# Optimization experiments

Measured on AMD Instinct MI355X. Metric: run time of the kernel, lower is better.

Reference implementation:

```python
import jax, jax.numpy as jnp
import numpy as np

S, O, J, B = 16, 8, 32, 4096
HID, OUT_HID = 240, 512
P1, P2 = 0.5, 0.65  # Bayesian (concrete) dropout probabilities, mid of [0.5, 0.8]


def setup_inputs() -> dict:
    key = jax.random.key(0)
    ks = jax.random.split(key, 20)
    sc = 0.05
    return {
        "y_t": jax.random.normal(ks[0], (B, O), jnp.float32),
        "x_filtered_prev": jax.random.normal(ks[1], (B, S), jnp.float32),
        "F": jax.random.normal(ks[2], (S, S), jnp.float32) * sc,
        "H": jax.random.normal(ks[3], (O, S), jnp.float32) * sc,
        "W_fc_in": jax.random.normal(ks[4], (HID, 2 * S + 2 * O), jnp.float32) * sc,
        "b_fc_in": jax.random.normal(ks[5], (HID,), jnp.float32) * sc,
        "W_ih": jax.random.normal(ks[6], (3 * HID, HID), jnp.float32) * sc,
        "W_hh": jax.random.normal(ks[7], (3 * HID, HID), jnp.float32) * sc,
        "b_ih": jax.random.normal(ks[8], (3 * HID,), jnp.float32) * sc,
        "b_hh": jax.random.normal(ks[9], (3 * HID,), jnp.float32) * sc,
        "W_out1": jax.random.normal(ks[10], (OUT_HID, HID), jnp.float32) * sc,
        "b_out1": jax.random.normal(ks[11], (OUT_HID,), jnp.float32) * sc,
        "W_out2": jax.random.normal(ks[12], (S * O, OUT_HID), jnp.float32) * sc,
        "b_out2": jax.random.normal(ks[13], (S * O,), jnp.float32) * sc,
        "h_init": jax.random.normal(ks[14], (HID,), jnp.float32),
        "u1": jax.random.uniform(ks[15], (J, B, HID), jnp.float32),
        "u2": jax.random.uniform(ks[16], (J, B, OUT_HID), jnp.float32),
    }


def reference(y_t, x_filtered_prev, F, H, W_fc_in, b_fc_in, W_ih, W_hh, b_ih,
              b_hh, W_out1, b_out1, W_out2, b_out2, h_init, u1, u2):
    # --- first step of step_StateBayesianKalmanNet, fully batched over (J, B) ---
    x_pred = x_filtered_prev @ F.T                 # f(x): [B,S]
    y_pred = x_pred @ H.T                          # h(x): [B,O]
    state_inno = x_filtered_prev - x_pred          # x_filt_prev - x_pred_prev
    innovation = y_t - y_pred
    diff_state = jnp.zeros_like(x_filtered_prev)   # first step: x_prev - x_prev_prev = 0
    diff_obs = y_t - y_pred                        # y_prev = h(x_pred) on first step

    feats = jnp.concatenate([state_inno, innovation, diff_state, diff_obs], -1)  # [B,48]
    x_in = jax.nn.relu(feats @ W_fc_in.T + b_fc_in)                              # [B,HID]
    mask1 = (u1 > P1).astype(x_in.dtype) / (1.0 - P1)                            # [J,B,HID]
    x_in = x_in[None] * mask1                                                    # Bayesian dropout sample j

    # single GRU cell step (torch gate order r,z,n), h_prev = h_init broadcast
    gx = x_in @ W_ih.T + b_ih                                                    # [J,B,3H]
    gh = h_init @ W_hh.T + b_hh                                                  # [3H]
    xr, xz, xn = jnp.split(gx, 3, axis=-1)
    hr, hz, hn = jnp.split(gh, 3, axis=-1)
    r = jax.nn.sigmoid(xr + hr)
    z = jax.nn.sigmoid(xz + hz)
    n = jnp.tanh(xn + r * hn)
    h_new = (1.0 - z) * n + z * h_init                                           # [J,B,HID]

    o1 = jax.nn.relu(h_new @ W_out1.T + b_out1)                                  # [J,B,OUT_HID]
    mask2 = (u2 > P2).astype(o1.dtype) / (1.0 - P2)
    o1 = o1 * mask2
    K_vec = o1 @ W_out2.T + b_out2                                               # [J,B,S*O]
    K = K_vec.reshape(J, B, S, O)

    correction = jnp.einsum('jbso,bo->jbs', K, innovation)
    x_filt = x_pred[None] + correction                                           # [J,B,S]
    ensemble = jnp.transpose(x_filt, (1, 0, 2))                                  # [B,J,S]
    final_x = ensemble.mean(axis=1)
    final_P_diag = ensemble.var(axis=1, ddof=1)                                  # torch unbiased var

    # concrete-dropout regularization (entropy of the two dropout gates, mean over J)
    reg = -(P1 * jnp.log(P1) + (1 - P1) * jnp.log(1 - P1)) \
          - (P2 * jnp.log(P2) + (1 - P2) * jnp.log(1 - P2))
    reg = jnp.asarray(reg, final_x.dtype)

    return final_x, final_P_diag, reg, ensemble
```

## Files before the change

kernel.cpp:

```cpp
#include <hip/hip_runtime.h>
#include <hip/hip_bf16.h>
#include <math.h>

#define S_DIM 16
#define O_DIM 8
#define J_DIM 32
#define B_DIM 4096
#define HID 240
#define OHID 512

typedef __attribute__((ext_vector_type(8))) short bf16x8;
typedef __attribute__((ext_vector_type(4))) float f32x4;
#define MFMA16(a,b,c) __builtin_amdgcn_mfma_f32_16x16x32_bf16((a),(b),(c),0,0,0)

static __device__ __forceinline__ float fast_rcp(float x) { return __builtin_amdgcn_rcpf(x); }
static __device__ __forceinline__ float fast_sigmoid(float x) {
    return fast_rcp(1.0f + __expf(-x));
}
static __device__ __forceinline__ float fast_tanh(float x) {
    float t = __expf(2.0f * x);
    return 1.0f - 2.0f * fast_rcp(t + 1.0f);
}

#define WS_XPRED   0
#define WS_INNO    (WS_XPRED + B_DIM*S_DIM)
#define WS_FEATS   (WS_INNO + B_DIM*O_DIM)
#define WS_XIN0    (WS_FEATS + B_DIM*48)
#define WS_GH      (WS_XIN0 + B_DIM*HID)
#define WS_WB_OFF  ((WS_GH + 960) * 4)

#define OUT_X      0
#define OUT_P      (B_DIM*S_DIM)
#define OUT_REG    (2*B_DIM*S_DIM)
#define OUT_ENS    (2*B_DIM*S_DIM + 1)

__global__ void k_aux_pre(const float* __restrict__ W_ih, const float* __restrict__ W_hh,
                          const float* __restrict__ b_ih, const float* __restrict__ b_hh,
                          const float* __restrict__ h_init,
                          const float* __restrict__ W_o1, const float* __restrict__ W_o2,
                          __hip_bfloat16* __restrict__ Wihb, __hip_bfloat16* __restrict__ Wo1b,
                          __hip_bfloat16* __restrict__ Wo2b, float* __restrict__ ghb,
                          const float* __restrict__ y, const float* __restrict__ xprev,
                          const float* __restrict__ F, const float* __restrict__ Hm,
                          float* __restrict__ x_pred, float* __restrict__ inno,
                          float* __restrict__ feats)
{
    __shared__ float sF[256], sH[128];
    const int tid = threadIdx.x;
    if (blockIdx.x < 1536) {
        int t = blockIdx.x * 256 + tid;
        if (t < 196608) {
            int e = t & 7, l = (t >> 3) & 15, q = (t >> 7) & 3;
            int ks = (t >> 9) & 7, tile = t >> 12;
            int row = tile*16 + l, col = ks*32 + q*8 + e;
            float v = (row < 720 && col < 240) ? W_ih[row*240 + col] : 0.0f;
            Wihb[t] = __float2bfloat16(v);
        } else if (t < 196608 + 131072) {
            int u = t - 196608;
            int e = u & 7, l = (u >> 3) & 15, q = (u >> 7) & 3;
            int ks = (u >> 9) & 7, tile = u >> 12;
            int row = tile*16 + l, col = ks*32 + q*8 + e;
            float v = (col < 240) ? W_o1[row*240 + col] : 0.0f;
            Wo1b[u] = __float2bfloat16(v);
        } else if (t < 393216) {
            int u = t - 327680;
            int e = u & 7, l = (u >> 3) & 15, q = (u >> 7) & 3;
            int ks = (u >> 9) & 15, tile = u >> 13;
            int row = tile*16 + l, col = ks*32 + q*8 + e;
            Wo2b[u] = __float2bfloat16(W_o2[row*512 + col]);
        }
        if (t < 720) {
            float a = b_hh[t];
            const float* wr = W_hh + t*240;
            for (int k = 0; k < 240; k++) a = fmaf(h_init[k], wr[k], a);
            if (t < 480) {
                ghb[t] = b_ih[t] + a;
            } else {
                ghb[t] = b_ih[t];
                ghb[t + 240] = a;
            }
        }
        return;
    }
    sF[tid] = F[tid];
    if (tid < 128) sH[tid] = Hm[tid];
    __syncthreads();
    int b = (blockIdx.x - 1536) * 256 + tid;
    float xf[16], xp[16], inn[8];
    #pragma unroll
    for (int s = 0; s < 16; s++) xf[s] = xprev[b*16 + s];
    #pragma unroll
    for (int s = 0; s < 16; s++) {
        float a = 0.f;
        #pragma unroll
        for (int k = 0; k < 16; k++) a = fmaf(xf[k], sF[s*16 + k], a);
        xp[s] = a;
    }
    #pragma unroll
    for (int o = 0; o < 8; o++) {
        float a = 0.f;
        #pragma unroll
        for (int k = 0; k < 16; k++) a = fmaf(xp[k], sH[o*16 + k], a);
        inn[o] = y[b*8 + o] - a;
    }
    #pragma unroll
    for (int s = 0; s < 16; s++) x_pred[b*16 + s] = xp[s];
    #pragma unroll
    for (int o = 0; o < 8; o++) inno[b*8 + o] = inn[o];
    float* fb = feats + b*48;
    #pragma unroll
    for (int s = 0; s < 16; s++) fb[s] = xf[s] - xp[s];
    #pragma unroll
    for (int o = 0; o < 8; o++) fb[16 + o] = inn[o];
    #pragma unroll
    for (int s = 0; s < 16; s++) fb[24 + s] = 0.f;
    #pragma unroll
    for (int o = 0; o < 8; o++) fb[40 + o] = inn[o];
}

__global__ void k_pre_b(const float* __restrict__ feats, const float* __restrict__ Wfc,
                        const float* __restrict__ bfc, float* __restrict__ x_in0)
{
    int t = blockIdx.x * 256 + threadIdx.x;
    int b = t / 240, h = t - b*240;
    const float* fb = feats + b*48;
    const float* wr = Wfc + h*48;
    float a = bfc[h];
    #pragma unroll
    for (int k = 0; k < 48; k += 4) {
        const float4 f4 = *(const float4*)&fb[k];
        const float4 w4 = *(const float4*)&wr[k];
        a = fmaf(f4.x, w4.x, fmaf(f4.y, w4.y, fmaf(f4.z, w4.z, fmaf(f4.w, w4.w, a))));
    }
    x_in0[t] = fmaxf(a, 0.f);
}

#define XS_STRIDE 264
#define O1_STRIDE 520

__global__ __launch_bounds__(512, 2) void k_main(
    const float* __restrict__ x_in0, const float* __restrict__ u1,
    const float* __restrict__ u2,
    const __hip_bfloat16* __restrict__ Wihb, const float* __restrict__ ghb,
    const float* __restrict__ h_init,
    const __hip_bfloat16* __restrict__ Wo1b, const float* __restrict__ b_out1,
    const __hip_bfloat16* __restrict__ Wo2b, const float* __restrict__ b_out2,
    const float* __restrict__ x_pred, const float* __restrict__ inno,
    float* __restrict__ ens)
{
    __shared__ __align__(16) char smem[73728];
    __hip_bfloat16* Xs  = (__hip_bfloat16*)smem;
    __hip_bfloat16* Hs  = (__hip_bfloat16*)(smem + 33792);
    __hip_bfloat16* O1s = (__hip_bfloat16*)smem;
    unsigned int* Mbits = (unsigned int*)(smem + 67584);
    float* InnoS = (float*)(smem + 71680);

    const int tid = threadIdx.x;
    const int j  = blockIdx.x >> 6;
    const int b0 = (blockIdx.x & 63) << 6;

    {
        const float4* u2t = (const float4*)(u2 + ((size_t)(j*B_DIM + b0) << 9));
        const int sh = (tid & 7) * 4;
        #pragma unroll
        for (int it = 0; it < 16; ++it) {
            float4 q = u2t[tid + 512*it];
            unsigned int nib = (q.x > 0.65f ? 1u : 0u) | (q.y > 0.65f ? 2u : 0u)
                             | (q.z > 0.65f ? 4u : 0u) | (q.w > 0.65f ? 8u : 0u);
            unsigned int v = nib << sh;
            v |= __shfl_xor(v, 1);
            v |= __shfl_xor(v, 2);
            v |= __shfl_xor(v, 4);
            if ((tid & 7) == 0) Mbits[(tid >> 3) + 64*it] = v;
        }
    }

    {
        const float4* xt = (const float4*)(x_in0 + b0*240);
        const float4* ut = (const float4*)(u1 + (size_t)(j*B_DIM + b0)*240);
        #pragma unroll
        for (int it = 0; it < 8; ++it) {
            int idx = tid + 512*it;
            if (idx < 3840) {
                float4 xv = xt[idx];
                float4 uv = ut[idx];
                int i = idx / 60;
                int h = (idx - i*60) * 4;
                __align__(8) __hip_bfloat16 o[4];
                o[0] = __float2bfloat16(uv.x > 0.5f ? 2.0f*xv.x : 0.0f);
                o[1] = __float2bfloat16(uv.y > 0.5f ? 2.0f*xv.y : 0.0f);
                o[2] = __float2bfloat16(uv.z > 0.5f ? 2.0f*xv.z : 0.0f);
                o[3] = __float2bfloat16(uv.w > 0.5f ? 2.0f*xv.w : 0.0f);
                *(uint2*)&Xs[i*XS_STRIDE + h] = *(const uint2*)o;
            }
        }
    }
    if (tid < 256) {
        int row = tid >> 2, c = 240 + ((tid & 3) << 2);
        uint2 z = {0u, 0u};
        *(uint2*)&Xs[row*XS_STRIDE + c] = z;
        *(uint2*)&Hs[row*XS_STRIDE + c] = z;
    }
    InnoS[tid & 511] = inno[b0*8 + (tid & 511)];
    __syncthreads();

    const int wave = tid >> 6;
    const int l15  = tid & 15;
    const int quad = (tid >> 4) & 3;
    const f32x4 zero4 = {0.f, 0.f, 0.f, 0.f};
    const int fragoff = quad*128 + l15*8;

    #pragma unroll 1
    for (int sl = 0; sl < 2; ++sl) {
        const int t = wave + 8*sl;
        if (t < 15) {
            f32x4 aR[4], aZ[4], aN[4];
            #pragma unroll
            for (int m = 0; m < 4; ++m) { aR[m] = zero4; aZ[m] = zero4; aN[m] = zero4; }

            const __hip_bfloat16* wr = Wihb + t*4096 + fragoff;
            #pragma unroll
            for (int ks = 0; ks < 8; ++ks) {
                const int ko = ks*32 + quad*8;
                bf16x8 a[4];
                #pragma unroll
                for (int m = 0; m < 4; ++m)
                    a[m] = *(const bf16x8*)&Xs[(m*16 + l15)*XS_STRIDE + ko];
                bf16x8 br = *(const bf16x8*)&wr[ks*512];
                bf16x8 bz = *(const bf16x8*)&wr[61440 + ks*512];
                bf16x8 bn = *(const bf16x8*)&wr[122880 + ks*512];
                #pragma unroll
                for (int m = 0; m < 4; ++m) {
                    aR[m] = MFMA16(a[m], br, aR[m]);
                    aZ[m] = MFMA16(a[m], bz, aZ[m]);
                    aN[m] = MFMA16(a[m], bn, aN[m]);
                }
            }
            const int h = t*16 + l15;
            const float add_r = ghb[h],       add_z = ghb[240 + h];
            const float add_n = ghb[480 + h], mul_n = ghb[720 + h];
            const float hi = h_init[h];
            #pragma unroll
            for (int m = 0; m < 4; ++m)
                #pragma unroll
                for (int r = 0; r < 4; ++r) {
                    const int row = m*16 + quad*4 + r;
                    float rg = fast_sigmoid(aR[m][r] + add_r);
                    float zg = fast_sigmoid(aZ[m][r] + add_z);
                    float ng = fast_tanh(aN[m][r] + add_n + rg*mul_n);
                    Hs[row*XS_STRIDE + h] = __float2bfloat16(fmaf(zg, hi - ng, ng));
                }
        }
    }
    __syncthreads();

    {
        f32x4 acc2[4][4];
        #pragma unroll
        for (int it = 0; it < 4; ++it)
            #pragma unroll
            for (int m = 0; m < 4; ++m) acc2[it][m] = zero4;

        const __hip_bfloat16* w2 = Wo1b + wave*16384 + fragoff;
        #pragma unroll
        for (int ks = 0; ks < 8; ++ks) {
            bf16x8 a[4];
            const int ko = ks*32 + quad*8;
            #pragma unroll
            for (int m = 0; m < 4; ++m)
                a[m] = *(const bf16x8*)&Hs[(m*16 + l15)*XS_STRIDE + ko];
            #pragma unroll
            for (int it = 0; it < 4; ++it) {
                bf16x8 b = *(const bf16x8*)&w2[it*4096 + ks*512];
                #pragma unroll
                for (int m = 0; m < 4; ++m)
                    acc2[it][m] = MFMA16(a[m], b, acc2[it][m]);
            }
        }
        __syncthreads();
        const float inv35 = 1.0f/0.35f;
        #pragma unroll
        for (int it = 0; it < 4; ++it) {
            const int n = (wave*4 + it)*16 + l15;
            const float bb = b_out1[n];
            const int wbase = (wave*4 + it) >> 1;
            const int bitpos = ((it & 1) << 4) | l15;
            #pragma unroll
            for (int m = 0; m < 4; ++m)
                #pragma unroll
                for (int r = 0; r < 4; ++r) {
                    const int row = m*16 + quad*4 + r;
                    unsigned int mw = Mbits[row*16 + wbase];
                    float o = fmaxf(acc2[it][m][r] + bb, 0.0f);
                    o = ((mw >> bitpos) & 1u) ? o*inv35 : 0.0f;
                    O1s[row*O1_STRIDE + n] = __float2bfloat16(o);
                }
        }
    }
    __syncthreads();

    {
        const int n = wave*16 + l15;
        const float bo = b_out2[n];
        f32x4 acc3[4];
        #pragma unroll
        for (int m = 0; m < 4; ++m) { f32x4 v = {bo, bo, bo, bo}; acc3[m] = v; }

        const __hip_bfloat16* w3 = Wo2b + wave*8192 + fragoff;
        #pragma unroll
        for (int ks = 0; ks < 16; ++ks) {
            const int ko = ks*32 + quad*8;
            bf16x8 b = *(const bf16x8*)&w3[ks*512];
            #pragma unroll
            for (int m = 0; m < 4; ++m) {
                bf16x8 a = *(const bf16x8*)&O1s[(m*16 + l15)*O1_STRIDE + ko];
                acc3[m] = MFMA16(a, b, acc3[m]);
            }
        }
        const int s = n >> 3, o = n & 7;
        #pragma unroll
        for (int m = 0; m < 4; ++m)
            #pragma unroll
            for (int r = 0; r < 4; ++r) {
                const int row = m*16 + quad*4 + r;
                float v = acc3[m][r] * InnoS[row*8 + o];
                v += __shfl_xor(v, 1);
                v += __shfl_xor(v, 2);
                v += __shfl_xor(v, 4);
                if (o == 0)
                    ens[((b0 + row)*J_DIM + j)*16 + s] = x_pred[(b0 + row)*16 + s] + v;
            }
    }
}

__global__ void k_final(const float* __restrict__ ens, float* __restrict__ out)
{
    int t = blockIdx.x * 256 + threadIdx.x;
    int b = t >> 4, s = t & 15;
    float v[32];
    #pragma unroll
    for (int jj = 0; jj < 32; jj++) v[jj] = ens[(b*32 + jj)*16 + s];
    float m = 0.f;
    #pragma unroll
    for (int jj = 0; jj < 32; jj++) m += v[jj];
    m *= (1.0f/32.0f);
    float var = 0.f;
    #pragma unroll
    for (int jj = 0; jj < 32; jj++) { float d = v[jj] - m; var = fmaf(d, d, var); }
    var *= (1.0f/31.0f);
    out[OUT_X + t] = m;
    out[OUT_P + t] = var;
    if (t == 0) out[OUT_REG] = 1.3405938195945778f;
}

extern "C" void kernel_launch(void* const* d_in, const int* in_sizes, int n_in,
                              void* d_out, int out_size, void* d_ws, size_t ws_size,
                              hipStream_t stream)
{
    (void)in_sizes; (void)n_in; (void)out_size; (void)ws_size;
    const float* y_t    = (const float*)d_in[0];
    const float* xprev  = (const float*)d_in[1];
    const float* F      = (const float*)d_in[2];
    const float* Hm     = (const float*)d_in[3];
    const float* Wfc    = (const float*)d_in[4];
    const float* bfc    = (const float*)d_in[5];
    const float* W_ih   = (const float*)d_in[6];
    const float* W_hh   = (const float*)d_in[7];
    const float* b_ih   = (const float*)d_in[8];
    const float* b_hh   = (const float*)d_in[9];
    const float* W_o1   = (const float*)d_in[10];
    const float* b_o1   = (const float*)d_in[11];
    const float* W_o2   = (const float*)d_in[12];
    const float* b_o2   = (const float*)d_in[13];
    const float* h_init = (const float*)d_in[14];
    const float* u1     = (const float*)d_in[15];
    const float* u2     = (const float*)d_in[16];

    float* out = (float*)d_out;
    float* ws  = (float*)d_ws;
    float* x_pred = ws + WS_XPRED;
    float* inno   = ws + WS_INNO;
    float* feats  = ws + WS_FEATS;
    float* x_in0  = ws + WS_XIN0;
    float* ghb    = ws + WS_GH;
    __hip_bfloat16* Wihb = (__hip_bfloat16*)((char*)d_ws + WS_WB_OFF);
    __hip_bfloat16* Wo1b = Wihb + 768*256;
    __hip_bfloat16* Wo2b = Wo1b + 512*256;
    float* ens    = out + OUT_ENS;

    k_aux_pre<<<dim3(1552), dim3(256), 0, stream>>>(W_ih, W_hh, b_ih, b_hh, h_init,
                                                    W_o1, W_o2, Wihb, Wo1b, Wo2b, ghb,
                                                    y_t, xprev, F, Hm, x_pred, inno, feats);
    k_pre_b<<<dim3(3840), dim3(256), 0, stream>>>(feats, Wfc, bfc, x_in0);
    k_main<<<dim3(2048), dim3(512), 0, stream>>>(x_in0, u1, u2, Wihb, ghb, h_init,
                                                 Wo1b, b_o1, Wo2b, b_o2,
                                                 x_pred, inno, ens);
    k_final<<<dim3(256), dim3(256), 0, stream>>>(ens, out);
}
```

Baseline: 753.8 us.

## Pre-pack dropout masks into bitmasks in a separate kernel and store x_in as bf16

```diff
diff --git a/kernel.cpp b/kernel.cpp
--- a/kernel.cpp
+++ b/kernel.cpp
@@ -25,9 +25,8 @@
 #define WS_XPRED   0
 #define WS_INNO    (WS_XPRED + B_DIM*S_DIM)
 #define WS_FEATS   (WS_INNO + B_DIM*O_DIM)
-#define WS_XIN0    (WS_FEATS + B_DIM*48)
-#define WS_GH      (WS_XIN0 + B_DIM*HID)
-#define WS_WB_OFF  ((WS_GH + 960) * 4)
+#define WS_GH      (WS_FEATS + B_DIM*48)
+#define WS_BYTE    ((WS_GH + 960) * 4)
 
 #define OUT_X      0
 #define OUT_P      (B_DIM*S_DIM)
@@ -119,7 +118,7 @@
 }
 
 __global__ void k_pre_b(const float* __restrict__ feats, const float* __restrict__ Wfc,
-                        const float* __restrict__ bfc, float* __restrict__ x_in0)
+                        const float* __restrict__ bfc, __hip_bfloat16* __restrict__ xb)
 {
     int t = blockIdx.x * 256 + threadIdx.x;
     int b = t / 240, h = t - b*240;
@@ -132,15 +131,62 @@
         const float4 w4 = *(const float4*)&wr[k];
         a = fmaf(f4.x, w4.x, fmaf(f4.y, w4.y, fmaf(f4.z, w4.z, fmaf(f4.w, w4.w, a))));
     }
-    x_in0[t] = fmaxf(a, 0.f);
+    xb[t] = __float2bfloat16(2.0f * fmaxf(a, 0.f));
+}
+
+__global__ __launch_bounds__(256) void k_pack(
+    const float* __restrict__ u1, const float* __restrict__ u2,
+    unsigned int* __restrict__ M1, unsigned int* __restrict__ M2)
+{
+    const int tid = threadIdx.x;
+    const size_t f0 = (size_t)blockIdx.x * 64;
+    {
+        const float4* u1t = (const float4*)(u1 + f0 * 240);
+        #pragma unroll
+        for (int it = 0; it < 4; ++it) {
+            int task = tid + 256*it;
+            int row = task >> 4, t = task & 15;
+            unsigned int bits = 0;
+            if (t < 15) {
+                const float4* p = u1t + row*60 + t*4;
+                #pragma unroll
+                for (int q = 0; q < 4; ++q) {
+                    float4 v = p[q];
+                    bits |= (v.x > 0.5f ? 1u : 0u) << (q*4);
+                    bits |= (v.y > 0.5f ? 2u : 0u) << (q*4);
+                    bits |= (v.z > 0.5f ? 4u : 0u) << (q*4);
+                    bits |= (v.w > 0.5f ? 8u : 0u) << (q*4);
+                }
+            }
+            unsigned int other = __shfl_xor(bits, 1);
+            if ((t & 1) == 0)
+                M1[(f0 + row)*8 + (t >> 1)] = bits | (other << 16);
+        }
+    }
+    {
+        const float4* u2t = (const float4*)(u2 + f0 * 512);
+        const int sh = (tid & 7) * 4;
+        #pragma unroll 8
+        for (int it = 0; it < 32; ++it) {
+            int idx = tid + 256*it;
+            float4 q = u2t[idx];
+            unsigned int nib = (q.x > 0.65f ? 1u : 0u) | (q.y > 0.65f ? 2u : 0u)
+                             | (q.z > 0.65f ? 4u : 0u) | (q.w > 0.65f ? 8u : 0u);
+            unsigned int v = nib << sh;
+            v |= __shfl_xor(v, 1);
+            v |= __shfl_xor(v, 2);
+            v |= __shfl_xor(v, 4);
+            if ((tid & 7) == 0) M2[f0*16 + (idx >> 3)] = v;
+        }
+    }
 }
 
 #define XS_STRIDE 264
 #define O1_STRIDE 520
 
 __global__ __launch_bounds__(512, 2) void k_main(
-    const float* __restrict__ x_in0, const float* __restrict__ u1,
-    const float* __restrict__ u2,
+    const __hip_bfloat16* __restrict__ xb,
+    const unsigned int* __restrict__ M1, const unsigned int* __restrict__ M2,
     const __hip_bfloat16* __restrict__ Wihb, const float* __restrict__ ghb,
     const float* __restrict__ h_init,
     const __hip_bfloat16* __restrict__ Wo1b, const float* __restrict__ b_out1,
@@ -158,40 +204,28 @@
     const int tid = threadIdx.x;
     const int j  = blockIdx.x >> 6;
     const int b0 = (blockIdx.x & 63) << 6;
+    const size_t f0 = (size_t)j * B_DIM + b0;
+
+    Mbits[tid]       = M2[f0*16 + tid];
+    Mbits[tid + 512] = M2[f0*16 + tid + 512];
 
     {
-        const float4* u2t = (const float4*)(u2 + ((size_t)(j*B_DIM + b0) << 9));
-        const int sh = (tid & 7) * 4;
-        #pragma unroll
-        for (int it = 0; it < 16; ++it) {
-            float4 q = u2t[tid + 512*it];
-            unsigned int nib = (q.x > 0.65f ? 1u : 0u) | (q.y > 0.65f ? 2u : 0u)
-                             | (q.z > 0.65f ? 4u : 0u) | (q.w > 0.65f ? 8u : 0u);
-            unsigned int v = nib << sh;
-            v |= __shfl_xor(v, 1);
-            v |= __shfl_xor(v, 2);
-            v |= __shfl_xor(v, 4);
-            if ((tid & 7) == 0) Mbits[(tid >> 3) + 64*it] = v;
-        }
-    }
-
-    {
-        const float4* xt = (const float4*)(x_in0 + b0*240);
-        const float4* ut = (const float4*)(u1 + (size_t)(j*B_DIM + b0)*240);
-        #pragma unroll
-        for (int it = 0; it < 8; ++it) {
+        #pragma unroll
+        for (int it = 0; it < 4; ++it) {
             int idx = tid + 512*it;
-            if (idx < 3840) {
-                float4 xv = xt[idx];
-                float4 uv = ut[idx];
-                int i = idx / 60;
-                int h = (idx - i*60) * 4;
-                __align__(8) __hip_bfloat16 o[4];
-                o[0] = __float2bfloat16(uv.x > 0.5f ? 2.0f*xv.x : 0.0f);
-                o[1] = __float2bfloat16(uv.y > 0.5f ? 2.0f*xv.y : 0.0f);
-                o[2] = __float2bfloat16(uv.z > 0.5f ? 2.0f*xv.z : 0.0f);
-                o[3] = __float2bfloat16(uv.w > 0.5f ? 2.0f*xv.w : 0.0f);
-                *(uint2*)&Xs[i*XS_STRIDE + h] = *(const uint2*)o;
+            if (idx < 1920) {
+                int row = idx / 30;
+                int c8  = idx - row*30;
+                uint4 xv = *(const uint4*)(xb + ((size_t)(b0 + row)*240 + c8*8));
+                unsigned int m1w = M1[(f0 + row)*8 + (c8 >> 2)];
+                unsigned int bits = (m1w >> ((c8 & 3) * 8)) & 0xffu;
+                unsigned int w0 = xv.x, w1 = xv.y, w2 = xv.z, w3 = xv.w;
+                w0 &= ((bits & 1u) ? 0x0000ffffu : 0u) | ((bits & 2u)   ? 0xffff0000u : 0u);
+                w1 &= ((bits & 4u) ? 0x0000ffffu : 0u) | ((bits & 8u)   ? 0xffff0000u : 0u);
+                w2 &= ((bits & 16u)? 0x0000ffffu : 0u) | ((bits & 32u)  ? 0xffff0000u : 0u);
+                w3 &= ((bits & 64u)? 0x0000ffffu : 0u) | ((bits & 128u) ? 0xffff0000u : 0u);
+                uint4 o = {w0, w1, w2, w3};
+                *(uint4*)&Xs[row*XS_STRIDE + c8*8] = o;
             }
         }
     }
@@ -381,18 +415,22 @@
     float* x_pred = ws + WS_XPRED;
     float* inno   = ws + WS_INNO;
     float* feats  = ws + WS_FEATS;
-    float* x_in0  = ws + WS_XIN0;
     float* ghb    = ws + WS_GH;
-    __hip_bfloat16* Wihb = (__hip_bfloat16*)((char*)d_ws + WS_WB_OFF);
-    __hip_bfloat16* Wo1b = Wihb + 768*256;
-    __hip_bfloat16* Wo2b = Wo1b + 512*256;
+    char* pb = (char*)d_ws + WS_BYTE;
+    __hip_bfloat16* xb   = (__hip_bfloat16*)pb;
+    __hip_bfloat16* Wihb = (__hip_bfloat16*)(pb + 1966080);
+    __hip_bfloat16* Wo1b = Wihb + 196608;
+    __hip_bfloat16* Wo2b = Wo1b + 131072;
+    unsigned int*   M1   = (unsigned int*)(pb + 1966080 + 786432);
+    unsigned int*   M2   = M1 + 131072*8;
     float* ens    = out + OUT_ENS;
 
     k_aux_pre<<<dim3(1552), dim3(256), 0, stream>>>(W_ih, W_hh, b_ih, b_hh, h_init,
                                                     W_o1, W_o2, Wihb, Wo1b, Wo2b, ghb,
                                                     y_t, xprev, F, Hm, x_pred, inno, feats);
-    k_pre_b<<<dim3(3840), dim3(256), 0, stream>>>(feats, Wfc, bfc, x_in0);
-    k_main<<<dim3(2048), dim3(512), 0, stream>>>(x_in0, u1, u2, Wihb, ghb, h_init,
+    k_pre_b<<<dim3(3840), dim3(256), 0, stream>>>(feats, Wfc, bfc, xb);
+    k_pack<<<dim3(2048), dim3(256), 0, stream>>>(u1, u2, M1, M2);
+    k_main<<<dim3(2048), dim3(512), 0, stream>>>(xb, M1, M2, Wihb, ghb, h_init,
                                                  Wo1b, b_o1, Wo2b, b_o2,
                                                  x_pred, inno, ens);
     k_final<<<dim3(256), dim3(256), 0, stream>>>(ens, out);
```

New measurement: 707.5 us. -6.1%, faster.
